# Performance work log

Hardware: AMD Instinct MI355X
Metric: run time of the kernel (lower is better)

Reference implementation:

```python
import jax, jax.numpy as jnp
import numpy as np

B, H, V, T = 1024, 512, 2048, 32  # batch, hidden_size, output_size (vocab), max_len


def setup_inputs() -> dict:
    key = jax.random.key(0)
    ks = jax.random.split(key, 8)
    s = 1.0 / np.sqrt(H)  # torch LSTMCell/Linear init scale
    u = lambda k, shp: jax.random.uniform(k, shp, jnp.float32, -s, s)
    return {
        "encoder_hidden": jax.random.normal(ks[0], (B, H), jnp.float32),
        "encoder_cell": jax.random.normal(ks[1], (B, H), jnp.float32),
        "W_ih": u(ks[2], (4 * H, V)),   # LSTMCell(output_size -> hidden)
        "W_hh": u(ks[3], (4 * H, H)),
        "b_ih": u(ks[4], (4 * H,)),
        "b_hh": u(ks[5], (4 * H,)),
        "W_out": u(ks[6], (V, H)),      # Linear(hidden -> output_size)
        "b_out": u(ks[7], (V,)),
        "init_input": jnp.zeros((1, V), jnp.float32),
        "max_len": T,
        "eos_idx": 0,
    }


def reference(encoder_hidden, encoder_cell, W_ih, W_hh, b_ih, b_hh, W_out, b_out,
              init_input, max_len, eos_idx):
    batch = encoder_hidden.shape[0]
    vocab = W_out.shape[0]
    hid = encoder_hidden.shape[1]

    def lstm_cell(x, h, c):
        gates = x @ W_ih.T + b_ih + h @ W_hh.T + b_hh  # [B, 4H]
        i, f, g, o = jnp.split(gates, 4, axis=1)       # torch gate order i,f,g,o
        c_new = jax.nn.sigmoid(f) * c + jax.nn.sigmoid(i) * jnp.tanh(g)
        h_new = jax.nn.sigmoid(o) * jnp.tanh(c_new)
        return h_new, c_new

    def step(carry, _):
        h, c, x, mask = carry
        h, c = lstm_cell(x, h, c)
        logit = h @ W_out.T + b_out                    # [B, V]
        # eval / non-msg path: hard argmax one-hot
        predict = jax.nn.one_hot(jnp.argmax(logit, axis=1), vocab, dtype=mask.dtype)
        new_mask = mask * (1.0 - predict[:, eos_idx])  # [1, B]
        # embedding is None -> decoder_input = predict
        return (h, c, predict, new_mask), (predict, logit, mask)

    carry0 = (
        encoder_hidden,
        encoder_cell,
        jnp.broadcast_to(init_input, (batch, vocab)),
        jnp.ones((1, batch), jnp.float32),
    )
    _, (predicts, logits, masks) = jax.lax.scan(step, carry0, None, length=max_len)
    return predicts, logits, masks  # [T,B,V], [T,B,V], [T,1,B]
```

## Files before the change

kernel.cpp:

```cpp
#include <hip/hip_runtime.h>
#include <math.h>

#define B_ 1024
#define H_ 512
#define V_ 2048
#define T_ 32
#define G_ 2048
#define KP 1024
#define K3 1536
#define NC 24

#define A_SCALE 64.0f
#define B_SCALE 256.0f
#define SCALE_INV (1.0f / (64.0f * 256.0f))

typedef _Float16 f16x8 __attribute__((ext_vector_type(8)));
typedef float f32x4 __attribute__((ext_vector_type(4)));

__device__ __forceinline__ float sigmoidf_(float x) {
    return 1.0f / (1.0f + expf(-x));
}

__device__ __forceinline__ void stage16(const _Float16* g, _Float16* l) {
#if __has_builtin(__builtin_amdgcn_global_load_lds)
    __builtin_amdgcn_global_load_lds(
        (const __attribute__((address_space(1))) void*)g,
        (__attribute__((address_space(3))) void*)l, 16, 0, 0);
#else
    *(uint4*)l = *(const uint4*)g;
#endif
}

__device__ __forceinline__ void wgbar() { asm volatile("s_barrier" ::: "memory"); }

__global__ __launch_bounds__(256) void gemm1_fused(
    const _Float16* __restrict__ Hin,
    const _Float16* __restrict__ Wg,
    const float* __restrict__ bsum,
    const float* __restrict__ g0,
    const float* __restrict__ W_ihT,
    const float* __restrict__ W_ih,
    const int* __restrict__ idx,
    float* __restrict__ c,
    _Float16* __restrict__ Hout,
    int t, int modeA)
{
    __shared__ _Float16 As[2 * 2 * 128 * 32];
    __shared__ _Float16 Bs[2 * 2 * 64 * 32];
    const int tid = threadIdx.x;
    const int bm  = blockIdx.y * 128;
    const int bnj = blockIdx.x * 16;

    const int r   = tid >> 2;
    const int cc  = (tid & 3) * 8;
    const int gcB = ((r >> 4) << 9) + bnj + (r & 15);
    const _Float16* aSrc = Hin + (size_t)(bm + r) * KP + cc;
    const _Float16* bSrc = Wg  + (size_t)gcB * KP + cc;
    _Float16* aDst = As + tid * 8;
    _Float16* bDst = Bs + tid * 8;

    const int w    = tid >> 6;
    const int lane = tid & 63;
    const int l15  = lane & 15;
    const int kq   = lane >> 4;

    f32x4 acc[2][4];
#pragma unroll
    for (int mt = 0; mt < 2; ++mt)
#pragma unroll
        for (int q = 0; q < 4; ++q) acc[mt][q] = (f32x4){0.f, 0.f, 0.f, 0.f};

    auto STAGE = [&](int buf, int ch) {
        const int kk = ch * 64;
        const int aoff = (kk < 512) ? kk : kk - 512;
        const int boff = (kk < 1024) ? kk : kk - 1024;
#pragma unroll
        for (int ks = 0; ks < 2; ++ks) {
#pragma unroll
            for (int hh = 0; hh < 2; ++hh)
                stage16(aSrc + (size_t)hh * 64 * KP + aoff + ks * 32,
                        aDst + buf * 8192 + ks * 4096 + hh * 2048);
            stage16(bSrc + boff + ks * 32, bDst + buf * 4096 + ks * 2048);
        }
    };

    int cur = 0;
    STAGE(0, 0);
    for (int ch = 0; ch < NC; ++ch) {
        if (ch + 1 < NC) {
            STAGE(cur ^ 1, ch + 1);
            asm volatile("s_waitcnt vmcnt(6)" ::: "memory");
        } else {
            asm volatile("s_waitcnt vmcnt(0)" ::: "memory");
        }
        wgbar();
#pragma unroll
        for (int ks = 0; ks < 2; ++ks) {
            const _Float16* ab = As + cur * 8192 + ks * 4096;
            const _Float16* bb = Bs + cur * 4096 + ks * 2048;
            f16x8 a0 = *(const f16x8*)&ab[(w * 32 + l15) * 32 + kq * 8];
            f16x8 a1 = *(const f16x8*)&ab[(w * 32 + 16 + l15) * 32 + kq * 8];
#pragma unroll
            for (int q = 0; q < 4; ++q) {
                f16x8 b = *(const f16x8*)&bb[(q * 16 + l15) * 32 + kq * 8];
                acc[0][q] = __builtin_amdgcn_mfma_f32_16x16x32_f16(a0, b, acc[0][q], 0, 0, 0);
                acc[1][q] = __builtin_amdgcn_mfma_f32_16x16x32_f16(a1, b, acc[1][q], 0, 0, 0);
            }
        }
        wgbar();
        cur ^= 1;
    }

    const int j = bnj + l15;
    const float bs0 = bsum[j];
    const float bs1 = bsum[512 + j];
    const float bs2 = bsum[1024 + j];
    const float bs3 = bsum[1536 + j];
#pragma unroll
    for (int mt = 0; mt < 2; ++mt) {
#pragma unroll
        for (int rg = 0; rg < 4; ++rg) {
            const int row = bm + w * 32 + mt * 16 + kq * 4 + rg;
            float xg0, xg1, xg2, xg3;
            if (t == 0) {
                xg0 = g0[j]; xg1 = g0[512 + j]; xg2 = g0[1024 + j]; xg3 = g0[1536 + j];
            } else if (modeA) {
                const float* xr = W_ihT + (size_t)idx[row] * G_;
                xg0 = xr[j]; xg1 = xr[512 + j]; xg2 = xr[1024 + j]; xg3 = xr[1536 + j];
            } else {
                const int v = idx[row];
                xg0 = W_ih[(size_t)(j) * V_ + v];
                xg1 = W_ih[(size_t)(512 + j) * V_ + v];
                xg2 = W_ih[(size_t)(1024 + j) * V_ + v];
                xg3 = W_ih[(size_t)(1536 + j) * V_ + v];
            }
            const float gi = acc[mt][0][rg] * SCALE_INV + bs0 + xg0;
            const float gf = acc[mt][1][rg] * SCALE_INV + bs1 + xg1;
            const float gg = acc[mt][2][rg] * SCALE_INV + bs2 + xg2;
            const float go = acc[mt][3][rg] * SCALE_INV + bs3 + xg3;
            const float co = c[(size_t)row * H_ + j];
            const float cn = sigmoidf_(gf) * co + sigmoidf_(gi) * tanhf(gg);
            const float hn = sigmoidf_(go) * tanhf(cn);
            c[(size_t)row * H_ + j] = cn;
            const float hs = A_SCALE * hn;
            const _Float16 hi = (_Float16)hs;
            const _Float16 lo = (_Float16)(hs - (float)hi);
            Hout[(size_t)row * KP + j] = hi;
            Hout[(size_t)row * KP + 512 + j] = lo;
        }
    }
}

__global__ __launch_bounds__(256) void gemm2_fused(
    const _Float16* __restrict__ Hin,
    const _Float16* __restrict__ Wo,
    const float* __restrict__ b_out,
    float* __restrict__ logits,
    float* __restrict__ pval,
    int* __restrict__ pidx)
{
    __shared__ _Float16 As[2 * 2 * 64 * 32];
    __shared__ _Float16 Bs[2 * 2 * 128 * 32];
    const int tid = threadIdx.x;
    const int bm = blockIdx.y * 64;
    const int bn = blockIdx.x * 128;

    const int r  = tid >> 2;
    const int cc = (tid & 3) * 8;
    const _Float16* aSrc = Hin + (size_t)(bm + r) * KP + cc;
    const _Float16* bSrc = Wo  + (size_t)(bn + r) * KP + cc;
    _Float16* aDst = As + tid * 8;
    _Float16* bDst = Bs + tid * 8;

    const int w    = tid >> 6;
    const int wm   = w & 1;
    const int wn   = w >> 1;
    const int lane = tid & 63;
    const int l15  = lane & 15;
    const int kq   = lane >> 4;

    f32x4 acc[2][4];
#pragma unroll
    for (int mt = 0; mt < 2; ++mt)
#pragma unroll
        for (int nt = 0; nt < 4; ++nt) acc[mt][nt] = (f32x4){0.f, 0.f, 0.f, 0.f};

    auto STAGE = [&](int buf, int ch) {
        const int kk = ch * 64;
        const int aoff = (kk < 512) ? kk : kk - 512;
        const int boff = (kk < 1024) ? kk : kk - 1024;
#pragma unroll
        for (int ks = 0; ks < 2; ++ks) {
            stage16(aSrc + aoff + ks * 32, aDst + buf * 4096 + ks * 2048);
#pragma unroll
            for (int hh = 0; hh < 2; ++hh)
                stage16(bSrc + (size_t)hh * 64 * KP + boff + ks * 32,
                        bDst + buf * 8192 + ks * 4096 + hh * 2048);
        }
    };

    int cur = 0;
    STAGE(0, 0);
    for (int ch = 0; ch < NC; ++ch) {
        if (ch + 1 < NC) {
            STAGE(cur ^ 1, ch + 1);
            asm volatile("s_waitcnt vmcnt(6)" ::: "memory");
        } else {
            asm volatile("s_waitcnt vmcnt(0)" ::: "memory");
        }
        wgbar();
#pragma unroll
        for (int ks = 0; ks < 2; ++ks) {
            const _Float16* ab = As + cur * 4096 + ks * 2048;
            const _Float16* bb = Bs + cur * 8192 + ks * 4096;
            f16x8 a0 = *(const f16x8*)&ab[(wm * 32 + l15) * 32 + kq * 8];
            f16x8 a1 = *(const f16x8*)&ab[(wm * 32 + 16 + l15) * 32 + kq * 8];
#pragma unroll
            for (int nt = 0; nt < 4; ++nt) {
                f16x8 b = *(const f16x8*)&bb[(wn * 64 + nt * 16 + l15) * 32 + kq * 8];
                acc[0][nt] = __builtin_amdgcn_mfma_f32_16x16x32_f16(a0, b, acc[0][nt], 0, 0, 0);
                acc[1][nt] = __builtin_amdgcn_mfma_f32_16x16x32_f16(a1, b, acc[1][nt], 0, 0, 0);
            }
        }
        wgbar();
        cur ^= 1;
    }

    const int cb = bn + wn * 64;
    const int c0 = cb + l15, c1 = cb + 16 + l15, c2 = cb + 32 + l15, c3 = cb + 48 + l15;
    const float bo0 = b_out[c0], bo1 = b_out[c1], bo2 = b_out[c2], bo3 = b_out[c3];
    const int cid = blockIdx.x * 4 + wn * 2;
#pragma unroll
    for (int mt = 0; mt < 2; ++mt) {
#pragma unroll
        for (int rg = 0; rg < 4; ++rg) {
            const int row = bm + wm * 32 + mt * 16 + kq * 4 + rg;
            const float v0 = acc[mt][0][rg] * SCALE_INV + bo0;
            const float v1 = acc[mt][1][rg] * SCALE_INV + bo1;
            const float v2 = acc[mt][2][rg] * SCALE_INV + bo2;
            const float v3 = acc[mt][3][rg] * SCALE_INV + bo3;
            float* lrow = logits + (size_t)row * V_;
            lrow[c0] = v0; lrow[c1] = v1; lrow[c2] = v2; lrow[c3] = v3;
            float bv; int bc;
            if (v1 > v0) { bv = v1; bc = c1; } else { bv = v0; bc = c0; }
#pragma unroll
            for (int off = 1; off < 16; off <<= 1) {
                const float ov = __shfl_xor(bv, off, 64);
                const int   oc = __shfl_xor(bc, off, 64);
                if (ov > bv || (ov == bv && oc < bc)) { bv = ov; bc = oc; }
            }
            if (l15 == 0) { pval[row * 64 + cid] = bv; pidx[row * 64 + cid] = bc; }
            if (v3 > v2) { bv = v3; bc = c3; } else { bv = v2; bc = c2; }
#pragma unroll
            for (int off = 1; off < 16; off <<= 1) {
                const float ov = __shfl_xor(bv, off, 64);
                const int   oc = __shfl_xor(bc, off, 64);
                if (ov > bv || (ov == bv && oc < bc)) { bv = ov; bc = oc; }
            }
            if (l15 == 0) { pval[row * 64 + cid + 1] = bv; pidx[row * 64 + cid + 1] = bc; }
        }
    }
}

__global__ __launch_bounds__(256) void finalize_step(
    const float* __restrict__ pval, const int* __restrict__ pidx,
    float* __restrict__ predicts_t, float* __restrict__ masks_t,
    float* __restrict__ mask, int* __restrict__ idx,
    const int* __restrict__ eos_idx)
{
    const int row  = blockIdx.x * 4 + (threadIdx.x >> 6);
    const int lane = threadIdx.x & 63;
    float bv = pval[row * 64 + lane];
    int   bc = pidx[row * 64 + lane];
#pragma unroll
    for (int off = 1; off < 64; off <<= 1) {
        const float ov = __shfl_xor(bv, off, 64);
        const int   oc = __shfl_xor(bc, off, 64);
        if (ov > bv || (ov == bv && oc < bc)) { bv = ov; bc = oc; }
    }
    if (lane == 0) {
        idx[row] = bc;
        predicts_t[(size_t)row * V_ + bc] = 1.0f;
        masks_t[row] = mask[row];
        if (bc == *eos_idx) mask[row] = 0.0f;
    }
}

__global__ __launch_bounds__(256) void prep_misc(
    const float* __restrict__ eh, const float* __restrict__ ec,
    const float* __restrict__ b_ih, const float* __restrict__ b_hh,
    _Float16* __restrict__ hA, float* __restrict__ c,
    float* __restrict__ bsum, float* __restrict__ mask)
{
    const int gid = blockIdx.x * 256 + threadIdx.x;
    const int row = gid >> 9;
    const int j   = gid & 511;
    const float x = eh[gid];
    c[gid] = ec[gid];
    const float xs = A_SCALE * x;
    const _Float16 hi = (_Float16)xs;
    const _Float16 lo = (_Float16)(xs - (float)hi);
    hA[(size_t)row * KP + j] = hi;
    hA[(size_t)row * KP + 512 + j] = lo;
    if (gid < G_) bsum[gid] = b_ih[gid] + b_hh[gid];
    if (gid < B_) mask[gid] = 1.0f;
}

__global__ __launch_bounds__(256) void prep_w(
    const float* __restrict__ W_hh, const float* __restrict__ W_out,
    _Float16* __restrict__ Wg, _Float16* __restrict__ Wo)
{
    const int gid = blockIdx.x * 256 + threadIdx.x;
    const int sel = gid >> 20;
    const int i   = gid & 1048575;
    const int n   = i >> 9;
    const int k   = i & 511;
    const float ws = (sel ? W_out[i] : W_hh[i]) * B_SCALE;
    const _Float16 hi = (_Float16)ws;
    const _Float16 lo = (_Float16)(ws - (float)hi);
    _Float16* dst = sel ? Wo : Wg;
    dst[(size_t)n * KP + k] = hi;
    dst[(size_t)n * KP + 512 + k] = lo;
}

__global__ __launch_bounds__(256) void transpose2048(const float* __restrict__ in,
                                                     float* __restrict__ out)
{
    __shared__ float tile[32][33];
    const int bx = blockIdx.x * 32;
    const int by = blockIdx.y * 32;
    const int tx = threadIdx.x & 31;
    const int ty = threadIdx.x >> 5;
#pragma unroll
    for (int i = 0; i < 32; i += 8)
        tile[ty + i][tx] = in[(size_t)(by + ty + i) * V_ + bx + tx];
    __syncthreads();
#pragma unroll
    for (int i = 0; i < 32; i += 8)
        out[(size_t)(bx + ty + i) * G_ + by + tx] = tile[tx][ty + i];
}

__global__ __launch_bounds__(256) void g0_kernel(const float* __restrict__ init_input,
                                                 const float* __restrict__ W_ih,
                                                 float* __restrict__ g0)
{
    const int gc   = blockIdx.x * 4 + (threadIdx.x >> 6);
    const int lane = threadIdx.x & 63;
    float acc = 0.0f;
    for (int v = lane; v < V_; v += 64) acc += init_input[v] * W_ih[(size_t)gc * V_ + v];
#pragma unroll
    for (int off = 32; off > 0; off >>= 1) acc += __shfl_down(acc, off, 64);
    if (lane == 0) g0[gc] = acc;
}

extern "C" void kernel_launch(void* const* d_in, const int* in_sizes, int n_in,
                              void* d_out, int out_size, void* d_ws, size_t ws_size,
                              hipStream_t stream) {
    const float* enc_h      = (const float*)d_in[0];
    const float* enc_c      = (const float*)d_in[1];
    const float* W_ih       = (const float*)d_in[2];
    const float* W_hh       = (const float*)d_in[3];
    const float* b_ih       = (const float*)d_in[4];
    const float* b_hh       = (const float*)d_in[5];
    const float* W_out      = (const float*)d_in[6];
    const float* b_out      = (const float*)d_in[7];
    const float* init_input = (const float*)d_in[8];
    const int*   eos_idx    = (const int*)d_in[10];

    float* out      = (float*)d_out;
    float* predicts = out;
    float* logits   = out + (size_t)T_ * B_ * V_;
    float* masks    = out + 2 * (size_t)T_ * B_ * V_;

    size_t off = 0;
    auto alloc = [&](size_t bytes) {
        void* p = (char*)d_ws + off;
        off += (bytes + 255) & ~(size_t)255;
        return p;
    };
    _Float16* Wg   = (_Float16*)alloc((size_t)G_ * KP * 2);
    _Float16* Wo   = (_Float16*)alloc((size_t)V_ * KP * 2);
    _Float16* hA   = (_Float16*)alloc((size_t)B_ * KP * 2);
    _Float16* hB   = (_Float16*)alloc((size_t)B_ * KP * 2);
    float*    c    = (float*)alloc((size_t)B_ * H_ * 4);
    float*    pval = (float*)alloc((size_t)B_ * 64 * 4);
    int*      pidx = (int*)alloc((size_t)B_ * 64 * 4);
    float*    g0   = (float*)alloc((size_t)G_ * 4);
    float*    bsum = (float*)alloc((size_t)G_ * 4);
    float*    mask = (float*)alloc((size_t)B_ * 4);
    int*      idx  = (int*)alloc((size_t)B_ * 4);
    float*    W_ihT = (float*)((char*)d_ws + off);
    const int modeA = (off + (size_t)V_ * G_ * 4) <= ws_size;

    hipMemsetAsync(predicts, 0, (size_t)T_ * B_ * V_ * sizeof(float), stream);
    prep_misc<<<(B_ * H_) / 256, 256, 0, stream>>>(enc_h, enc_c, b_ih, b_hh, hA, c, bsum, mask);
    prep_w<<<(2 * G_ * H_) / 256, 256, 0, stream>>>(W_hh, W_out, Wg, Wo);
    g0_kernel<<<G_ / 4, 256, 0, stream>>>(init_input, W_ih, g0);
    if (modeA)
        transpose2048<<<dim3(64, 64), 256, 0, stream>>>(W_ih, W_ihT);

    for (int t = 0; t < T_; ++t) {
        const _Float16* hin = (t & 1) ? hB : hA;
        _Float16*      hout = (t & 1) ? hA : hB;
        gemm1_fused<<<dim3(32, 8), 256, 0, stream>>>(
            hin, Wg, bsum, g0, W_ihT, W_ih, idx, c, hout, t, modeA);
        gemm2_fused<<<dim3(16, 16), 256, 0, stream>>>(
            hout, Wo, b_out, logits + (size_t)t * B_ * V_, pval, pidx);
        finalize_step<<<256, 256, 0, stream>>>(
            pval, pidx, predicts + (size_t)t * B_ * V_, masks + (size_t)t * B_,
            mask, idx, eos_idx);
    }
}
```

Measured before the change: 2.255 ms.

## Use 512-thread blocks in both GEMMs, splitting gate tiles across twice the waves

Both per-step GEMM kernels now launch 8 waves per block instead of 4, and each wave keeps half as many accumulator tiles. In gemm1 the four LSTM gates are split across wave pairs, so the accumulators are exchanged through LDS before the fused cell update. Each thread also issues fewer staging loads. With only 256 blocks per GEMM, this is meant to put more waves on each CU to hide memory and MFMA latency. The cost is an extra LDS round-trip and barrier in the gemm1 epilogue, and higher per-block resource use.

```diff
diff --git a/kernel.cpp b/kernel.cpp
--- a/kernel.cpp
+++ b/kernel.cpp
@@ -33,7 +33,8 @@
 
 __device__ __forceinline__ void wgbar() { asm volatile("s_barrier" ::: "memory"); }
 
-__global__ __launch_bounds__(256) void gemm1_fused(
+
+__global__ __launch_bounds__(512, 2) void gemm1_fused(
     const _Float16* __restrict__ Hin,
     const _Float16* __restrict__ Wg,
     const float* __restrict__ bsum,
@@ -51,37 +52,34 @@
     const int bm  = blockIdx.y * 128;
     const int bnj = blockIdx.x * 16;
 
-    const int r   = tid >> 2;
-    const int cc  = (tid & 3) * 8;
-    const int gcB = ((r >> 4) << 9) + bnj + (r & 15);
-    const _Float16* aSrc = Hin + (size_t)(bm + r) * KP + cc;
-    const _Float16* bSrc = Wg  + (size_t)gcB * KP + cc;
+    const int rB  = (tid & 255) >> 2;
+    const int gcB = ((rB >> 4) << 9) + bnj + (rB & 15);
+    const _Float16* aSrc = Hin + (size_t)(bm + (tid >> 2)) * KP + (tid & 3) * 8;
+    const _Float16* bSrc = Wg  + (size_t)gcB * KP + (tid >> 8) * 32 + (tid & 3) * 8;
     _Float16* aDst = As + tid * 8;
-    _Float16* bDst = Bs + tid * 8;
+    _Float16* bDst = Bs + (tid >> 8) * 2048 + (tid & 255) * 8;
 
     const int w    = tid >> 6;
+    const int wr   = w >> 1;
+    const int wc   = w & 1;
     const int lane = tid & 63;
     const int l15  = lane & 15;
     const int kq   = lane >> 4;
 
-    f32x4 acc[2][4];
+    f32x4 acc[2][2];
 #pragma unroll
     for (int mt = 0; mt < 2; ++mt)
 #pragma unroll
-        for (int q = 0; q < 4; ++q) acc[mt][q] = (f32x4){0.f, 0.f, 0.f, 0.f};
+        for (int g = 0; g < 2; ++g) acc[mt][g] = (f32x4){0.f, 0.f, 0.f, 0.f};
 
     auto STAGE = [&](int buf, int ch) {
         const int kk = ch * 64;
         const int aoff = (kk < 512) ? kk : kk - 512;
         const int boff = (kk < 1024) ? kk : kk - 1024;
 #pragma unroll
-        for (int ks = 0; ks < 2; ++ks) {
-#pragma unroll
-            for (int hh = 0; hh < 2; ++hh)
-                stage16(aSrc + (size_t)hh * 64 * KP + aoff + ks * 32,
-                        aDst + buf * 8192 + ks * 4096 + hh * 2048);
-            stage16(bSrc + boff + ks * 32, bDst + buf * 4096 + ks * 2048);
-        }
+        for (int ks = 0; ks < 2; ++ks)
+            stage16(aSrc + aoff + ks * 32, aDst + buf * 8192 + ks * 4096);
+        stage16(bSrc + boff, bDst + buf * 4096);
     };
 
     int cur = 0;
@@ -89,7 +87,7 @@
     for (int ch = 0; ch < NC; ++ch) {
         if (ch + 1 < NC) {
             STAGE(cur ^ 1, ch + 1);
-            asm volatile("s_waitcnt vmcnt(6)" ::: "memory");
+            asm volatile("s_waitcnt vmcnt(3)" ::: "memory");
         } else {
             asm volatile("s_waitcnt vmcnt(0)" ::: "memory");
         }
@@ -98,18 +96,34 @@
         for (int ks = 0; ks < 2; ++ks) {
             const _Float16* ab = As + cur * 8192 + ks * 4096;
             const _Float16* bb = Bs + cur * 4096 + ks * 2048;
-            f16x8 a0 = *(const f16x8*)&ab[(w * 32 + l15) * 32 + kq * 8];
-            f16x8 a1 = *(const f16x8*)&ab[(w * 32 + 16 + l15) * 32 + kq * 8];
-#pragma unroll
-            for (int q = 0; q < 4; ++q) {
-                f16x8 b = *(const f16x8*)&bb[(q * 16 + l15) * 32 + kq * 8];
-                acc[0][q] = __builtin_amdgcn_mfma_f32_16x16x32_f16(a0, b, acc[0][q], 0, 0, 0);
-                acc[1][q] = __builtin_amdgcn_mfma_f32_16x16x32_f16(a1, b, acc[1][q], 0, 0, 0);
+            f16x8 a0 = *(const f16x8*)&ab[(wr * 32 + l15) * 32 + kq * 8];
+            f16x8 a1 = *(const f16x8*)&ab[(wr * 32 + 16 + l15) * 32 + kq * 8];
+#pragma unroll
+            for (int g = 0; g < 2; ++g) {
+                f16x8 b = *(const f16x8*)&bb[((wc * 2 + g) * 16 + l15) * 32 + kq * 8];
+                acc[0][g] = __builtin_amdgcn_mfma_f32_16x16x32_f16(a0, b, acc[0][g], 0, 0, 0);
+                acc[1][g] = __builtin_amdgcn_mfma_f32_16x16x32_f16(a1, b, acc[1][g], 0, 0, 0);
             }
         }
         wgbar();
         cur ^= 1;
     }
+
+    float* sc    = (float*)As;
+    float* sc_go = sc;
+    float* sc_if = sc + 2048;
+#pragma unroll
+    for (int rg = 0; rg < 4; ++rg) {
+        const int rl = wr * 16 + kq * 4 + rg;
+        if (wc == 1) {
+            sc_go[(rl * 16 + l15) * 2 + 0] = acc[0][0][rg];
+            sc_go[(rl * 16 + l15) * 2 + 1] = acc[0][1][rg];
+        } else {
+            sc_if[(rl * 16 + l15) * 2 + 0] = acc[1][0][rg];
+            sc_if[(rl * 16 + l15) * 2 + 1] = acc[1][1][rg];
+        }
+    }
+    __syncthreads();
 
     const int j = bnj + l15;
     const float bs0 = bsum[j];
@@ -117,41 +131,49 @@
     const float bs2 = bsum[1024 + j];
     const float bs3 = bsum[1536 + j];
 #pragma unroll
-    for (int mt = 0; mt < 2; ++mt) {
-#pragma unroll
-        for (int rg = 0; rg < 4; ++rg) {
-            const int row = bm + w * 32 + mt * 16 + kq * 4 + rg;
-            float xg0, xg1, xg2, xg3;
-            if (t == 0) {
-                xg0 = g0[j]; xg1 = g0[512 + j]; xg2 = g0[1024 + j]; xg3 = g0[1536 + j];
-            } else if (modeA) {
-                const float* xr = W_ihT + (size_t)idx[row] * G_;
-                xg0 = xr[j]; xg1 = xr[512 + j]; xg2 = xr[1024 + j]; xg3 = xr[1536 + j];
-            } else {
-                const int v = idx[row];
-                xg0 = W_ih[(size_t)(j) * V_ + v];
-                xg1 = W_ih[(size_t)(512 + j) * V_ + v];
-                xg2 = W_ih[(size_t)(1024 + j) * V_ + v];
-                xg3 = W_ih[(size_t)(1536 + j) * V_ + v];
-            }
-            const float gi = acc[mt][0][rg] * SCALE_INV + bs0 + xg0;
-            const float gf = acc[mt][1][rg] * SCALE_INV + bs1 + xg1;
-            const float gg = acc[mt][2][rg] * SCALE_INV + bs2 + xg2;
-            const float go = acc[mt][3][rg] * SCALE_INV + bs3 + xg3;
-            const float co = c[(size_t)row * H_ + j];
-            const float cn = sigmoidf_(gf) * co + sigmoidf_(gi) * tanhf(gg);
-            const float hn = sigmoidf_(go) * tanhf(cn);
-            c[(size_t)row * H_ + j] = cn;
-            const float hs = A_SCALE * hn;
-            const _Float16 hi = (_Float16)hs;
-            const _Float16 lo = (_Float16)(hs - (float)hi);
-            Hout[(size_t)row * KP + j] = hi;
-            Hout[(size_t)row * KP + 512 + j] = lo;
-        }
-    }
-}
-
-__global__ __launch_bounds__(256) void gemm2_fused(
+    for (int rg = 0; rg < 4; ++rg) {
+        const int rl  = wr * 16 + kq * 4 + rg;
+        const int row = bm + wr * 32 + wc * 16 + kq * 4 + rg;
+        float ai, af, ag, ao;
+        if (wc == 0) {
+            ai = acc[0][0][rg]; af = acc[0][1][rg];
+            ag = sc_go[(rl * 16 + l15) * 2 + 0];
+            ao = sc_go[(rl * 16 + l15) * 2 + 1];
+        } else {
+            ai = sc_if[(rl * 16 + l15) * 2 + 0];
+            af = sc_if[(rl * 16 + l15) * 2 + 1];
+            ag = acc[1][0][rg]; ao = acc[1][1][rg];
+        }
+        float xg0, xg1, xg2, xg3;
+        if (t == 0) {
+            xg0 = g0[j]; xg1 = g0[512 + j]; xg2 = g0[1024 + j]; xg3 = g0[1536 + j];
+        } else if (modeA) {
+            const float* xr = W_ihT + (size_t)idx[row] * G_;
+            xg0 = xr[j]; xg1 = xr[512 + j]; xg2 = xr[1024 + j]; xg3 = xr[1536 + j];
+        } else {
+            const int v = idx[row];
+            xg0 = W_ih[(size_t)(j) * V_ + v];
+            xg1 = W_ih[(size_t)(512 + j) * V_ + v];
+            xg2 = W_ih[(size_t)(1024 + j) * V_ + v];
+            xg3 = W_ih[(size_t)(1536 + j) * V_ + v];
+        }
+        const float gi = ai * SCALE_INV + bs0 + xg0;
+        const float gf = af * SCALE_INV + bs1 + xg1;
+        const float gg = ag * SCALE_INV + bs2 + xg2;
+        const float go = ao * SCALE_INV + bs3 + xg3;
+        const float co = c[(size_t)row * H_ + j];
+        const float cn = sigmoidf_(gf) * co + sigmoidf_(gi) * tanhf(gg);
+        const float hn = sigmoidf_(go) * tanhf(cn);
+        c[(size_t)row * H_ + j] = cn;
+        const float hs = A_SCALE * hn;
+        const _Float16 hi = (_Float16)hs;
+        const _Float16 lo = (_Float16)(hs - (float)hi);
+        Hout[(size_t)row * KP + j] = hi;
+        Hout[(size_t)row * KP + 512 + j] = lo;
+    }
+}
+
+__global__ __launch_bounds__(512, 2) void gemm2_fused(
     const _Float16* __restrict__ Hin,
     const _Float16* __restrict__ Wo,
     const float* __restrict__ b_out,
@@ -165,11 +187,9 @@
     const int bm = blockIdx.y * 64;
     const int bn = blockIdx.x * 128;
 
-    const int r  = tid >> 2;
-    const int cc = (tid & 3) * 8;
-    const _Float16* aSrc = Hin + (size_t)(bm + r) * KP + cc;
-    const _Float16* bSrc = Wo  + (size_t)(bn + r) * KP + cc;
-    _Float16* aDst = As + tid * 8;
+    const _Float16* aSrc = Hin + (size_t)(bm + ((tid & 255) >> 2)) * KP + (tid & 3) * 8;
+    const _Float16* bSrc = Wo  + (size_t)(bn + (tid >> 2)) * KP + (tid & 3) * 8;
+    _Float16* aDst = As + (tid >> 8) * 2048 + (tid & 255) * 8;
     _Float16* bDst = Bs + tid * 8;
 
     const int w    = tid >> 6;
@@ -179,24 +199,20 @@
     const int l15  = lane & 15;
     const int kq   = lane >> 4;
 
-    f32x4 acc[2][4];
+    f32x4 acc[2][2];
 #pragma unroll
     for (int mt = 0; mt < 2; ++mt)
 #pragma unroll
-        for (int nt = 0; nt < 4; ++nt) acc[mt][nt] = (f32x4){0.f, 0.f, 0.f, 0.f};
+        for (int nt = 0; nt < 2; ++nt) acc[mt][nt] = (f32x4){0.f, 0.f, 0.f, 0.f};
 
     auto STAGE = [&](int buf, int ch) {
         const int kk = ch * 64;
         const int aoff = (kk < 512) ? kk : kk - 512;
         const int boff = (kk < 1024) ? kk : kk - 1024;
-#pragma unroll
-        for (int ks = 0; ks < 2; ++ks) {
-            stage16(aSrc + aoff + ks * 32, aDst + buf * 4096 + ks * 2048);
-#pragma unroll
-            for (int hh = 0; hh < 2; ++hh)
-                stage16(bSrc + (size_t)hh * 64 * KP + boff + ks * 32,
-                        bDst + buf * 8192 + ks * 4096 + hh * 2048);
-        }
+        stage16(aSrc + aoff + (tid >> 8) * 32, aDst + buf * 4096);
+#pragma unroll
+        for (int ks = 0; ks < 2; ++ks)
+            stage16(bSrc + boff + ks * 32, bDst + buf * 8192 + ks * 4096);
     };
 
     int cur = 0;
@@ -204,7 +220,7 @@
     for (int ch = 0; ch < NC; ++ch) {
         if (ch + 1 < NC) {
             STAGE(cur ^ 1, ch + 1);
-            asm volatile("s_waitcnt vmcnt(6)" ::: "memory");
+            asm volatile("s_waitcnt vmcnt(3)" ::: "memory");
         } else {
             asm volatile("s_waitcnt vmcnt(0)" ::: "memory");
         }
@@ -216,8 +232,8 @@
             f16x8 a0 = *(const f16x8*)&ab[(wm * 32 + l15) * 32 + kq * 8];
             f16x8 a1 = *(const f16x8*)&ab[(wm * 32 + 16 + l15) * 32 + kq * 8];
 #pragma unroll
-            for (int nt = 0; nt < 4; ++nt) {
-                f16x8 b = *(const f16x8*)&bb[(wn * 64 + nt * 16 + l15) * 32 + kq * 8];
+            for (int nt = 0; nt < 2; ++nt) {
+                f16x8 b = *(const f16x8*)&bb[((wn * 32 + nt * 16) + l15) * 32 + kq * 8];
                 acc[0][nt] = __builtin_amdgcn_mfma_f32_16x16x32_f16(a0, b, acc[0][nt], 0, 0, 0);
                 acc[1][nt] = __builtin_amdgcn_mfma_f32_16x16x32_f16(a1, b, acc[1][nt], 0, 0, 0);
             }
@@ -226,10 +242,11 @@
         cur ^= 1;
     }
 
-    const int cb = bn + wn * 64;
-    const int c0 = cb + l15, c1 = cb + 16 + l15, c2 = cb + 32 + l15, c3 = cb + 48 + l15;
-    const float bo0 = b_out[c0], bo1 = b_out[c1], bo2 = b_out[c2], bo3 = b_out[c3];
-    const int cid = blockIdx.x * 4 + wn * 2;
+    const int c0 = bn + wn * 32 + l15;
+    const int c1 = c0 + 16;
+    const float bo0 = b_out[c0];
+    const float bo1 = b_out[c1];
+    const int cid = blockIdx.x * 4 + wn;
 #pragma unroll
     for (int mt = 0; mt < 2; ++mt) {
 #pragma unroll
@@ -237,10 +254,8 @@
             const int row = bm + wm * 32 + mt * 16 + kq * 4 + rg;
             const float v0 = acc[mt][0][rg] * SCALE_INV + bo0;
             const float v1 = acc[mt][1][rg] * SCALE_INV + bo1;
-            const float v2 = acc[mt][2][rg] * SCALE_INV + bo2;
-            const float v3 = acc[mt][3][rg] * SCALE_INV + bo3;
             float* lrow = logits + (size_t)row * V_;
-            lrow[c0] = v0; lrow[c1] = v1; lrow[c2] = v2; lrow[c3] = v3;
+            lrow[c0] = v0; lrow[c1] = v1;
             float bv; int bc;
             if (v1 > v0) { bv = v1; bc = c1; } else { bv = v0; bc = c0; }
 #pragma unroll
@@ -250,14 +265,6 @@
                 if (ov > bv || (ov == bv && oc < bc)) { bv = ov; bc = oc; }
             }
             if (l15 == 0) { pval[row * 64 + cid] = bv; pidx[row * 64 + cid] = bc; }
-            if (v3 > v2) { bv = v3; bc = c3; } else { bv = v2; bc = c2; }
-#pragma unroll
-            for (int off = 1; off < 16; off <<= 1) {
-                const float ov = __shfl_xor(bv, off, 64);
-                const int   oc = __shfl_xor(bc, off, 64);
-                if (ov > bv || (ov == bv && oc < bc)) { bv = ov; bc = oc; }
-            }
-            if (l15 == 0) { pval[row * 64 + cid + 1] = bv; pidx[row * 64 + cid + 1] = bc; }
         }
     }
 }
@@ -402,9 +409,9 @@
     for (int t = 0; t < T_; ++t) {
         const _Float16* hin = (t & 1) ? hB : hA;
         _Float16*      hout = (t & 1) ? hA : hB;
-        gemm1_fused<<<dim3(32, 8), 256, 0, stream>>>(
+        gemm1_fused<<<dim3(32, 8), 512, 0, stream>>>(
             hin, Wg, bsum, g0, W_ihT, W_ih, idx, c, hout, t, modeA);
-        gemm2_fused<<<dim3(16, 16), 256, 0, stream>>>(
+        gemm2_fused<<<dim3(16, 16), 512, 0, stream>>>(
             hout, Wo, b_out, logits + (size_t)t * B_ * V_, pval, pidx);
         finalize_step<<<256, 256, 0, stream>>>(
             pval, pidx, predicts + (size_t)t * B_ * V_, masks + (size_t)t * B_,
```

Result: faster. 1.923 ms (-14.7%).
